# Performance work log

Hardware: AMD Instinct MI355X
Metric: run time of the kernel (lower is better)

Reference implementation:

```python
import jax, jax.numpy as jnp
import numpy as np

SCORE_THRESHOLD = 0.01
NMS_THRESHOLD = 0.5
MAX_DETECTIONS = 100
PRE_NMS_TOPK = 200  # candidates kept per class before NMS (>= MAX_DETECTIONS)


def setup_inputs() -> dict:
    key = jax.random.key(0)
    kc, kcls, kw, kr, kt = jax.random.split(key, 5)
    B, N, C, R = 16, 100000, 30, 3
    # Build valid (x1,y1,x2,y2) boxes: random centers in a 512x512 image, sizes in [1,101].
    cxy = jax.random.uniform(kc, (B, N, 2), dtype=jnp.float32) * 512.0
    wh = jax.random.uniform(kw, (B, N, 2), dtype=jnp.float32) * 100.0 + 1.0
    boxes = jnp.concatenate([cxy - 0.5 * wh, cxy + 0.5 * wh], axis=-1)  # [B,N,4]
    classification = jax.random.uniform(kcls, (B, N, C), dtype=jnp.float32)
    rotation = jax.random.normal(kr, (B, N, R), dtype=jnp.float32)
    translation = jax.random.normal(kt, (B, N, 3), dtype=jnp.float32)
    return {"boxes": boxes, "classification": classification,
            "rotation": rotation, "translation": translation}


def _iou_matrix(b):  # b: [K,4] -> [K,K] pairwise IoU
    x1, y1, x2, y2 = b[:, 0], b[:, 1], b[:, 2], b[:, 3]
    area = jnp.maximum(x2 - x1, 0.0) * jnp.maximum(y2 - y1, 0.0)
    xx1 = jnp.maximum(x1[:, None], x1[None, :])
    yy1 = jnp.maximum(y1[:, None], y1[None, :])
    xx2 = jnp.minimum(x2[:, None], x2[None, :])
    yy2 = jnp.minimum(y2[:, None], y2[None, :])
    inter = jnp.maximum(xx2 - xx1, 0.0) * jnp.maximum(yy2 - yy1, 0.0)
    union = area[:, None] + area[None, :] - inter
    return inter / jnp.maximum(union, 1e-8)


def _nms_one_class(scores, boxes):
    # scores: [N], boxes: [N,4] -> (kept_scores [K], source_indices [K])
    masked = jnp.where(scores > SCORE_THRESHOLD, scores, -jnp.inf)
    top_s, top_i = jax.lax.top_k(masked, PRE_NMS_TOPK)
    cand = boxes[top_i]                      # [K,4], already sorted by score desc
    iou = _iou_matrix(cand)                  # [K,K]
    valid = jnp.isfinite(top_s)
    rng = jnp.arange(PRE_NMS_TOPK)

    def body(i, keep):
        suppress = (iou[i] > NMS_THRESHOLD) & (rng > i) & keep[i]
        return keep & ~suppress

    keep = jax.lax.fori_loop(0, PRE_NMS_TOPK, body, valid)
    return jnp.where(keep, top_s, -jnp.inf), top_i


def reference(boxes, classification, rotation, translation):
    B, N, C = classification.shape

    def per_image(bx, cls, rot, tr):
        # Per-class score threshold + NMS, vectorized over classes.
        s, idx = jax.vmap(lambda c: _nms_one_class(cls[:, c], bx))(jnp.arange(C))
        labels = jnp.broadcast_to(jnp.arange(C)[:, None], s.shape)
        s, idx, labels = s.reshape(-1), idx.reshape(-1), labels.reshape(-1)
        # Global top-k over all (class, kept-box) pairs.
        top_s, sel = jax.lax.top_k(s, MAX_DETECTIONS)
        fidx, flab = idx[sel], labels[sel]
        valid = jnp.isfinite(top_s)
        out_boxes = jnp.where(valid[:, None], bx[fidx], -1.0)
        out_scores = jnp.where(valid, top_s, -1.0)
        out_labels = jnp.where(valid, flab, -1).astype(jnp.int32)
        out_rot = jnp.where(valid[:, None], rot[fidx], -1.0)
        out_tr = jnp.where(valid[:, None], tr[fidx], -1.0)
        return out_boxes, out_scores, out_labels, out_rot, out_tr

    return jax.vmap(per_image)(boxes, classification, rotation, translation)
```

## Files before the change

### kernel.cpp

```cpp
#include <hip/hip_runtime.h>
#include <math.h>

typedef unsigned long long u64;

#define BATCH 16
#define NBOX 100000
#define NCLS 30
#define K 200
#define MAXDET 100
#define SCORE_THR 0.01f
#define NMS_THR 0.5f
#define T0 0.995f

#define ELEM_PER_BATCH (NBOX * NCLS)
#define CAP 1024
#define CHUNKS 48
#define VEC_PER_CHUNK 15625
#define LDS_CAP 48

#define OFF_COLL   0ull
#define OFF_CNT    (OFF_COLL + (size_t)BATCH*NCLS*CAP*8)
#define OFF_WSI    (OFF_CNT + 512*4)
#define OFF_MERGE  (OFF_WSI + (size_t)BATCH*NCLS*K*4)

__global__ __launch_bounds__(512) void collect_kernel(const float* __restrict__ cls,
                                                      int* __restrict__ cnt,
                                                      u64* __restrict__ coll) {
  const int b = blockIdx.x / CHUNKS;
  const int chunk = blockIdx.x % CHUNKS;
  const int tid = threadIdx.x;

  __shared__ u64 lbuf[NCLS][LDS_CAP];
  __shared__ int lcnt[NCLS];
  __shared__ int lbase[NCLS];

  if (tid < NCLS) lcnt[tid] = 0;
  __syncthreads();

  const int vbase = chunk * VEC_PER_CHUNK;
  const float4* p = (const float4*)(cls + (size_t)b * ELEM_PER_BATCH) + vbase;
  for (int i = tid; i < VEC_PER_CHUNK; i += 512) {
    float4 v = p[i];
    float m = fmaxf(fmaxf(v.x, v.y), fmaxf(v.z, v.w));
    if (m > T0) {
      float vv[4] = {v.x, v.y, v.z, v.w};
      #pragma unroll
      for (int j = 0; j < 4; ++j) {
        float f = vv[j];
        if (f > T0) {
          int e = (vbase + i) * 4 + j;
          int c = e % NCLS;
          int n = e / NCLS;
          int pos = atomicAdd(&lcnt[c], 1);
          if (pos < LDS_CAP)
            lbuf[c][pos] = ((u64)__float_as_uint(f) << 32) | (unsigned)(~(unsigned)n);
        }
      }
    }
  }
  __syncthreads();

  if (tid < NCLS) {
    int m = lcnt[tid];
    int stored = (m < LDS_CAP) ? m : LDS_CAP;
    int bump = (m > LDS_CAP) ? 1000000 : 0;
    int base = atomicAdd(&cnt[b * NCLS + tid], m + bump);
    lbase[tid] = base;
    lcnt[tid] = stored;
  }
  __syncthreads();

  for (int t = tid; t < NCLS * LDS_CAP; t += 512) {
    int c = t / LDS_CAP, s = t - (t / LDS_CAP) * LDS_CAP;
    if (s < lcnt[c]) {
      int slot = lbase[c] + s;
      if (slot < CAP)
        coll[(size_t)(b * NCLS + c) * CAP + slot] = lbuf[c][s];
    }
  }
}

__global__ __launch_bounds__(512) void fused_sort_nms_kernel(
    const u64* __restrict__ coll, const int* __restrict__ cnt,
    const float* __restrict__ cls, const float* __restrict__ boxes,
    int* __restrict__ ws_i, u64* __restrict__ merged) {
  const int bc = blockIdx.x;
  const int b = bc / NCLS, c = bc % NCLS;
  const int tid = threadIdx.x;

  __shared__ u64 arr[CAP];
  __shared__ float sx1[K], sy1[K], sx2[K], sy2[K], sarea[K], ss[K];
  __shared__ int sidx[K];
  __shared__ unsigned mask[K][8];
  __shared__ unsigned keepw[8];
  __shared__ int s_surv;
  __shared__ u64 comb[256];
  __shared__ unsigned eqbuf[512];
  __shared__ unsigned s_pref, s_mask, s_krem, s_takeall;
  __shared__ unsigned s_cntgt, s_cnteq;

  const int ct = cnt[bc];
  const bool bad = (ct < K) || (ct > CAP);
  if (!bad) {
    for (int i = tid; i < CAP; i += 512)
      arr[i] = (i < ct) ? coll[(size_t)bc * CAP + i] : 0ull;
    for (int k = 2; k <= CAP; k <<= 1) {
      for (int j = k >> 1; j > 0; j >>= 1) {
        __syncthreads();
        for (int i = tid; i < CAP; i += 512) {
          int l = i ^ j;
          if (l > i) {
            u64 a = arr[i], bb = arr[l];
            bool up = ((i & k) == 0);
            if (up ? (a < bb) : (a > bb)) { arr[i] = bb; arr[l] = a; }
          }
        }
      }
    }
    __syncthreads();
    for (int r = tid; r < K; r += 512) {
      u64 e = arr[r];
      float s = (e != 0ull) ? __uint_as_float((unsigned)(e >> 32)) : -INFINITY;
      int idx = (e != 0ull) ? (int)(~(unsigned)e) : 0;
      ss[r] = s; sidx[r] = idx;
      ws_i[bc * K + r] = idx;
    }
  } else {
    unsigned (*hist)[256] = (unsigned (*)[256])arr;
    const int wv = tid >> 6;
    if (tid == 0) { s_pref = 0u; s_mask = 0u; s_krem = K; s_takeall = 0u; }
    __syncthreads();
    const float* col = cls + (size_t)b * NBOX * NCLS + c;

    for (int pass = 0; pass < 4; ++pass) {
      if (s_takeall) break;
      const int shift = 24 - 8 * pass;
      for (int i = tid; i < 8 * 256; i += 512) ((unsigned*)hist)[i] = 0u;
      __syncthreads();
      const unsigned pref = s_pref, msk = s_mask;
      for (int n = tid; n < NBOX; n += 512) {
        float v = col[(size_t)n * NCLS];
        if (v > SCORE_THR) {
          unsigned key = __float_as_uint(v);
          if ((key & msk) == pref)
            atomicAdd(&hist[wv][(key >> shift) & 0xFFu], 1u);
        }
      }
      __syncthreads();
      if (tid < 256) {
        unsigned t2 = 0;
        for (int w = 0; w < 8; ++w) t2 += hist[w][tid];
        hist[0][tid] = t2;
      }
      __syncthreads();
      if (tid == 0) {
        unsigned krem = s_krem, cum = 0; int dsel = -1;
        for (int d = 255; d >= 0; --d) {
          unsigned cc = hist[0][d];
          if (cum + cc >= krem) { dsel = d; break; }
          cum += cc;
        }
        if (dsel < 0) s_takeall = 1u;
        else {
          s_krem = krem - cum;
          s_pref = pref | ((unsigned)dsel << shift);
          s_mask = msk | (0xFFu << shift);
        }
      }
      __syncthreads();
    }

    if (tid == 0) { s_cntgt = 0u; s_cnteq = 0u; }
    __syncthreads();
    const unsigned pivot = s_pref;
    const unsigned takeall = s_takeall;

    for (int n = tid; n < NBOX; n += 512) {
      float v = col[(size_t)n * NCLS];
      if (v > SCORE_THR) {
        unsigned key = __float_as_uint(v);
        if (takeall || key > pivot) {
          unsigned pos = atomicAdd(&s_cntgt, 1u);
          if (pos < 256u)
            comb[pos] = ((u64)key << 32) | (unsigned)(~(unsigned)n);
        } else if (key == pivot) {
          unsigned pos = atomicAdd(&s_cnteq, 1u);
          if (pos < 512u) eqbuf[pos] = (unsigned)n;
        }
      }
    }
    __syncthreads();
    const unsigned cntgt = (s_cntgt < 256u) ? s_cntgt : 256u;
    const unsigned cnteq = (s_cnteq < 512u) ? s_cnteq : 512u;
    unsigned need = 0;
    if (!takeall) {
      need = (cntgt < (unsigned)K) ? ((unsigned)K - cntgt) : 0u;
      if (need > cnteq) need = cnteq;
    }
    for (int i = tid; i < 512; i += 512)
      if ((unsigned)i >= cnteq) eqbuf[i] = 0xFFFFFFFFu;
    for (int k = 2; k <= 512; k <<= 1) {
      for (int j = k >> 1; j > 0; j >>= 1) {
        __syncthreads();
        {
          int i = tid, l = i ^ j;
          if (l > i) {
            unsigned a = eqbuf[i], bb = eqbuf[l];
            bool up = ((i & k) == 0);
            if (up ? (a > bb) : (a < bb)) { eqbuf[i] = bb; eqbuf[l] = a; }
          }
        }
      }
    }
    __syncthreads();
    for (int t = tid; t < (int)need; t += 512)
      comb[cntgt + t] = ((u64)pivot << 32) | (unsigned)(~eqbuf[t]);
    const unsigned M = cntgt + need;
    for (int i = tid; i < 256; i += 512)
      if ((unsigned)i >= M) comb[i] = 0ull;
    for (int k = 2; k <= 256; k <<= 1) {
      for (int j = k >> 1; j > 0; j >>= 1) {
        __syncthreads();
        if (tid < 256) {
          int i = tid, l = i ^ j;
          if (l > i) {
            u64 a = comb[i], bb = comb[l];
            bool up = ((i & k) == 0);
            if (up ? (a < bb) : (a > bb)) { comb[i] = bb; comb[l] = a; }
          }
        }
      }
    }
    __syncthreads();
    if (tid < K) {
      if ((unsigned)tid < M) {
        u64 e = comb[tid];
        ss[tid] = __uint_as_float((unsigned)(e >> 32));
        sidx[tid] = (int)(~(unsigned)e);
      } else {
        ss[tid] = -INFINITY;
        sidx[tid] = 0;
      }
      ws_i[bc * K + tid] = sidx[tid];
    }
  }
  for (int i = tid; i < K * 8; i += 512) ((unsigned*)mask)[i] = 0u;
  if (tid < 8) keepw[tid] = 0u;
  __syncthreads();

  for (int r = tid; r < K; r += 512) {
    float s = ss[r];
    bool valid = (s != -INFINITY);
    float x1 = 0.f, y1 = 0.f, x2 = 0.f, y2 = 0.f;
    if (valid) {
      const float* bp = boxes + ((size_t)b * NBOX + sidx[r]) * 4;
      x1 = bp[0]; y1 = bp[1]; x2 = bp[2]; y2 = bp[3];
      atomicOr(&keepw[r >> 5], 1u << (r & 31));
    }
    sx1[r] = x1; sy1[r] = y1; sx2[r] = x2; sy2[r] = y2;
    sarea[r] = fmaxf(x2 - x1, 0.f) * fmaxf(y2 - y1, 0.f);
  }
  __syncthreads();

  for (int t = tid; t < K * K; t += 512) {
    int i = t / K, j = t - i * K;
    if (j > i) {
      float xx1 = fmaxf(sx1[i], sx1[j]);
      float yy1 = fmaxf(sy1[i], sy1[j]);
      float xx2 = fminf(sx2[i], sx2[j]);
      float yy2 = fminf(sy2[i], sy2[j]);
      float inter = fmaxf(xx2 - xx1, 0.f) * fmaxf(yy2 - yy1, 0.f);
      float uni = sarea[i] + sarea[j] - inter;
      float iou = inter / fmaxf(uni, 1e-8f);
      if (iou > NMS_THR) atomicOr(&mask[i][j >> 5], 1u << (j & 31));
    }
  }
  __syncthreads();

  if (tid < 64) {
    int w = tid & 7;
    unsigned keep = keepw[w];
    for (int i = 0; i < K; ++i) {
      unsigned kw = __shfl(keep, i >> 5, 64);
      if ((kw >> (i & 31)) & 1u)
        keep &= ~mask[i][w];
    }
    if (tid < 8) keepw[tid] = keep;
  }
  __syncthreads();

  for (int r = tid; r < K; r += 512) {
    int w6 = r >> 5, bit = r & 31;
    if ((keepw[w6] >> bit) & 1u) {
      int pos = 0;
      #pragma unroll
      for (int w = 0; w < 7; ++w) {
        unsigned kw = keepw[w];
        if (w < w6) pos += __popc(kw);
        else if (w == w6) pos += __popc(kw & ((1u << bit) - 1u));
      }
      if (pos < 128) {
        unsigned ord = __float_as_uint(ss[r]) | 0x80000000u;
        merged[((size_t)b * 32 + c) * 128 + pos] =
          ((u64)ord << 32) | (unsigned)(~(unsigned)(c * K + r));
      }
    }
  }
  if (tid == 0) {
    int S = 0;
    #pragma unroll
    for (int w = 0; w < 7; ++w) S += __popc(keepw[w]);
    s_surv = S;
  }
  __syncthreads();
  for (int t = s_surv + tid; t < 128; t += 512)
    merged[((size_t)b * 32 + c) * 128 + t] = 0ull;
}

__global__ __launch_bounds__(1024) void merge_gather_kernel(
    const u64* __restrict__ merged, const int* __restrict__ ws_i,
    const float* __restrict__ boxes, const float* __restrict__ rot,
    const float* __restrict__ tr, float* __restrict__ out) {
  const int b = blockIdx.x;
  const int tid = threadIdx.x;
  __shared__ u64 W[4096];

  for (int t = tid; t < 4096; t += 1024) {
    int c = t >> 7, r = t & 127;
    W[t] = (c < NCLS) ? merged[((size_t)b * 32 + c) * 128 + r] : 0ull;
  }
  __syncthreads();

  int active = 4096;
  #pragma unroll
  for (int level = 0; level < 5; ++level) {
    int npairs = active >> 8;
    for (int t = tid; t < npairs * 64; t += 1024) {
      int p = t >> 6, q = t & 63;
      int i1 = p * 256 + 128 + q, i2 = p * 256 + 255 - q;
      u64 a = W[i1]; W[i1] = W[i2]; W[i2] = a;
    }
    __syncthreads();
    for (int j = 128; j > 0; j >>= 1) {
      for (int i = tid; i < active; i += 1024) {
        int l = i ^ j;
        if (l > i) {
          u64 a = W[i], bb = W[l];
          if (a < bb) { W[i] = bb; W[l] = a; }
        }
      }
      __syncthreads();
    }
    int half = active >> 1;
    u64 t0 = 0, t1 = 0;
    if (tid < half) t0 = W[(tid >> 7) * 256 + (tid & 127)];
    int t2i = tid + 1024;
    if (t2i < half) t1 = W[(t2i >> 7) * 256 + (t2i & 127)];
    __syncthreads();
    if (tid < half) W[tid] = t0;
    if (t2i < half) W[t2i] = t1;
    __syncthreads();
    active = half;
  }

  if (tid < MAXDET) {
    u64 key = W[tid];
    bool valid = (key != 0ull);
    float* ob  = out + ((size_t)b * MAXDET + tid) * 4;
    float* os  = out + (size_t)BATCH * MAXDET * 4 + b * MAXDET + tid;
    float* ol  = os + BATCH * MAXDET;
    float* orr = out + (size_t)BATCH * MAXDET * 6 + ((size_t)b * MAXDET + tid) * 3;
    float* ot  = orr + (size_t)BATCH * MAXDET * 3;

    if (valid) {
      unsigned f = ~(unsigned)key;
      int cl = (int)(f / K);
      float sc = __uint_as_float((unsigned)(key >> 32) & 0x7FFFFFFFu);
      int orig = ws_i[(size_t)b * NCLS * K + f];
      const float* bp = boxes + ((size_t)b * NBOX + orig) * 4;
      ob[0] = bp[0]; ob[1] = bp[1]; ob[2] = bp[2]; ob[3] = bp[3];
      *os = sc;
      *ol = (float)cl;
      const float* rp = rot + ((size_t)b * NBOX + orig) * 3;
      orr[0] = rp[0]; orr[1] = rp[1]; orr[2] = rp[2];
      const float* tp = tr + ((size_t)b * NBOX + orig) * 3;
      ot[0] = tp[0]; ot[1] = tp[1]; ot[2] = tp[2];
    } else {
      ob[0] = ob[1] = ob[2] = ob[3] = -1.f;
      *os = -1.f; *ol = -1.f;
      orr[0] = orr[1] = orr[2] = -1.f;
      ot[0] = ot[1] = ot[2] = -1.f;
    }
  }
}

extern "C" void kernel_launch(void* const* d_in, const int* in_sizes, int n_in,
                              void* d_out, int out_size, void* d_ws, size_t ws_size,
                              hipStream_t stream) {
  const float* boxes = (const float*)d_in[0];
  const float* cls   = (const float*)d_in[1];
  const float* rot   = (const float*)d_in[2];
  const float* tr    = (const float*)d_in[3];
  float* out = (float*)d_out;

  char* ws = (char*)d_ws;
  u64*   coll   = (u64*)(ws + OFF_COLL);
  int*   cnt    = (int*)(ws + OFF_CNT);
  int*   ws_i   = (int*)(ws + OFF_WSI);
  u64*   merged = (u64*)(ws + OFF_MERGE);

  hipMemsetAsync(cnt, 0, BATCH * NCLS * sizeof(int), stream);
  collect_kernel<<<BATCH * CHUNKS, 512, 0, stream>>>(cls, cnt, coll);
  fused_sort_nms_kernel<<<BATCH * NCLS, 512, 0, stream>>>(coll, cnt, cls, boxes,
                                                          ws_i, merged);
  merge_gather_kernel<<<BATCH, 1024, 0, stream>>>(merged, ws_i, boxes, rot, tr, out);
}
```

Baseline: 116.0 us.

## Fuse final merge into NMS kernel via last-block counter, restructure IoU loop

```diff
diff --git a/kernel.cpp b/kernel.cpp
--- a/kernel.cpp
+++ b/kernel.cpp
@@ -39,25 +39,33 @@
 
   const int vbase = chunk * VEC_PER_CHUNK;
   const float4* p = (const float4*)(cls + (size_t)b * ELEM_PER_BATCH) + vbase;
-  for (int i = tid; i < VEC_PER_CHUNK; i += 512) {
-    float4 v = p[i];
+
+  auto process = [&](float4 v, int idx) {
     float m = fmaxf(fmaxf(v.x, v.y), fmaxf(v.z, v.w));
     if (m > T0) {
       float vv[4] = {v.x, v.y, v.z, v.w};
       #pragma unroll
       for (int j = 0; j < 4; ++j) {
-        float f = vv[j];
-        if (f > T0) {
-          int e = (vbase + i) * 4 + j;
+        if (vv[j] > T0) {
+          int e = (vbase + idx) * 4 + j;
           int c = e % NCLS;
           int n = e / NCLS;
           int pos = atomicAdd(&lcnt[c], 1);
           if (pos < LDS_CAP)
-            lbuf[c][pos] = ((u64)__float_as_uint(f) << 32) | (unsigned)(~(unsigned)n);
-        }
-      }
-    }
-  }
+            lbuf[c][pos] = ((u64)__float_as_uint(vv[j]) << 32) | (unsigned)(~(unsigned)n);
+        }
+      }
+    }
+  };
+
+  int i = tid;
+  for (; i + 512 < VEC_PER_CHUNK; i += 1024) {
+    float4 a = p[i];
+    float4 b2 = p[i + 512];
+    process(a, i);
+    process(b2, i + 512);
+  }
+  if (i < VEC_PER_CHUNK) process(p[i], i);
   __syncthreads();
 
   if (tid < NCLS) {
@@ -83,19 +91,26 @@
 __global__ __launch_bounds__(512) void fused_sort_nms_kernel(
     const u64* __restrict__ coll, const int* __restrict__ cnt,
     const float* __restrict__ cls, const float* __restrict__ boxes,
-    int* __restrict__ ws_i, u64* __restrict__ merged) {
+    const float* __restrict__ rot, const float* __restrict__ tr,
+    int* __restrict__ ws_i, u64* __restrict__ merged,
+    int* __restrict__ bcnt, float* __restrict__ out) {
   const int bc = blockIdx.x;
   const int b = bc / NCLS, c = bc % NCLS;
   const int tid = threadIdx.x;
 
-  __shared__ u64 arr[CAP];
-  __shared__ float sx1[K], sy1[K], sx2[K], sy2[K], sarea[K], ss[K];
-  __shared__ int sidx[K];
-  __shared__ unsigned mask[K][8];
+  __shared__ char pool[32768] __attribute__((aligned(16)));
+  u64*      arr   = (u64*)pool;
+  float4*   sbox  = (float4*)(pool + 8192);
+  float*    sarea = (float*)(pool + 11392);
+  float*    ss    = (float*)(pool + 12192);
+  int*      sidx  = (int*)(pool + 12992);
+  unsigned (*mask)[8] = (unsigned (*)[8])(pool + 13792);
+  u64*      comb  = (u64*)(pool + 20192);
+  unsigned* eqbuf = (unsigned*)(pool + 22240);
+  u64*      W     = (u64*)pool;
+
   __shared__ unsigned keepw[8];
-  __shared__ int s_surv;
-  __shared__ u64 comb[256];
-  __shared__ unsigned eqbuf[512];
+  __shared__ int s_surv, s_last;
   __shared__ unsigned s_pref, s_mask, s_krem, s_takeall;
   __shared__ unsigned s_cntgt, s_cnteq;
 
@@ -204,7 +219,7 @@
         __syncthreads();
         {
           int i = tid, l = i ^ j;
-          if (l > i) {
+          if (l > i && i < 512) {
             unsigned a = eqbuf[i], bb = eqbuf[l];
             bool up = ((i & k) == 0);
             if (up ? (a > bb) : (a < bb)) { eqbuf[i] = bb; eqbuf[l] = a; }
@@ -244,6 +259,7 @@
       ws_i[bc * K + tid] = sidx[tid];
     }
   }
+
   for (int i = tid; i < K * 8; i += 512) ((unsigned*)mask)[i] = 0u;
   if (tid < 8) keepw[tid] = 0u;
   __syncthreads();
@@ -257,22 +273,35 @@
       x1 = bp[0]; y1 = bp[1]; x2 = bp[2]; y2 = bp[3];
       atomicOr(&keepw[r >> 5], 1u << (r & 31));
     }
-    sx1[r] = x1; sy1[r] = y1; sx2[r] = x2; sy2[r] = y2;
+    sbox[r] = make_float4(x1, y1, x2, y2);
     sarea[r] = fmaxf(x2 - x1, 0.f) * fmaxf(y2 - y1, 0.f);
   }
   __syncthreads();
 
-  for (int t = tid; t < K * K; t += 512) {
-    int i = t / K, j = t - i * K;
-    if (j > i) {
-      float xx1 = fmaxf(sx1[i], sx1[j]);
-      float yy1 = fmaxf(sy1[i], sy1[j]);
-      float xx2 = fminf(sx2[i], sx2[j]);
-      float yy2 = fminf(sy2[i], sy2[j]);
-      float inter = fmaxf(xx2 - xx1, 0.f) * fmaxf(yy2 - yy1, 0.f);
-      float uni = sarea[i] + sarea[j] - inter;
-      float iou = inter / fmaxf(uni, 1e-8f);
-      if (iou > NMS_THR) atomicOr(&mask[i][j >> 5], 1u << (j & 31));
+  {
+    const int jj = tid & 255;
+    const bool jvalid = (jj < K);
+    float jx1 = 0.f, jy1 = 0.f, jx2 = 0.f, jy2 = 0.f, ja = 0.f;
+    if (jvalid) {
+      float4 jb = sbox[jj];
+      jx1 = jb.x; jy1 = jb.y; jx2 = jb.z; jy2 = jb.w;
+      ja = sarea[jj];
+    }
+    #pragma unroll 4
+    for (int k2 = 0; k2 < K / 2; ++k2) {
+      int i = (tid >> 8) + 2 * k2;
+      float4 ib = sbox[i];
+      float ia = sarea[i];
+      if (jvalid && jj > i) {
+        float xx1 = fmaxf(ib.x, jx1);
+        float yy1 = fmaxf(ib.y, jy1);
+        float xx2 = fminf(ib.z, jx2);
+        float yy2 = fminf(ib.w, jy2);
+        float inter = fmaxf(xx2 - xx1, 0.f) * fmaxf(yy2 - yy1, 0.f);
+        float uni = ia + ja - inter;
+        float iou = inter / fmaxf(uni, 1e-8f);
+        if (iou > NMS_THR) atomicOr(&mask[i][jj >> 5], 1u << (jj & 31));
+      }
     }
   }
   __syncthreads();
@@ -315,34 +344,32 @@
   __syncthreads();
   for (int t = s_surv + tid; t < 128; t += 512)
     merged[((size_t)b * 32 + c) * 128 + t] = 0ull;
-}
-
-__global__ __launch_bounds__(1024) void merge_gather_kernel(
-    const u64* __restrict__ merged, const int* __restrict__ ws_i,
-    const float* __restrict__ boxes, const float* __restrict__ rot,
-    const float* __restrict__ tr, float* __restrict__ out) {
-  const int b = blockIdx.x;
-  const int tid = threadIdx.x;
-  __shared__ u64 W[4096];
-
-  for (int t = tid; t < 4096; t += 1024) {
-    int c = t >> 7, r = t & 127;
-    W[t] = (c < NCLS) ? merged[((size_t)b * 32 + c) * 128 + r] : 0ull;
+
+  __syncthreads();
+  __threadfence();
+  if (tid == 0)
+    s_last = (atomicAdd(&bcnt[b], 1) == NCLS - 1) ? 1 : 0;
+  __syncthreads();
+  if (!s_last) return;
+  __threadfence();
+
+  for (int t = tid; t < 4096; t += 512) {
+    int c2 = t >> 7, r = t & 127;
+    W[t] = (c2 < NCLS) ? merged[((size_t)b * 32 + c2) * 128 + r] : 0ull;
   }
   __syncthreads();
 
   int active = 4096;
-  #pragma unroll
   for (int level = 0; level < 5; ++level) {
     int npairs = active >> 8;
-    for (int t = tid; t < npairs * 64; t += 1024) {
+    for (int t = tid; t < npairs * 64; t += 512) {
       int p = t >> 6, q = t & 63;
       int i1 = p * 256 + 128 + q, i2 = p * 256 + 255 - q;
       u64 a = W[i1]; W[i1] = W[i2]; W[i2] = a;
     }
     __syncthreads();
     for (int j = 128; j > 0; j >>= 1) {
-      for (int i = tid; i < active; i += 1024) {
+      for (int i = tid; i < active; i += 512) {
         int l = i ^ j;
         if (l > i) {
           u64 a = W[i], bb = W[l];
@@ -352,13 +379,16 @@
       __syncthreads();
     }
     int half = active >> 1;
-    u64 t0 = 0, t1 = 0;
-    if (tid < half) t0 = W[(tid >> 7) * 256 + (tid & 127)];
-    int t2i = tid + 1024;
-    if (t2i < half) t1 = W[(t2i >> 7) * 256 + (t2i & 127)];
-    __syncthreads();
-    if (tid < half) W[tid] = t0;
-    if (t2i < half) W[t2i] = t1;
+    u64 v0 = 0, v1 = 0, v2 = 0, v3 = 0;
+    { int t = tid;        if (t < half) v0 = W[(t >> 7) * 256 + (t & 127)]; }
+    { int t = tid + 512;  if (t < half) v1 = W[(t >> 7) * 256 + (t & 127)]; }
+    { int t = tid + 1024; if (t < half) v2 = W[(t >> 7) * 256 + (t & 127)]; }
+    { int t = tid + 1536; if (t < half) v3 = W[(t >> 7) * 256 + (t & 127)]; }
+    __syncthreads();
+    { int t = tid;        if (t < half) W[t] = v0; }
+    { int t = tid + 512;  if (t < half) W[t] = v1; }
+    { int t = tid + 1024; if (t < half) W[t] = v2; }
+    { int t = tid + 1536; if (t < half) W[t] = v3; }
     __syncthreads();
     active = half;
   }
@@ -406,12 +436,13 @@
   char* ws = (char*)d_ws;
   u64*   coll   = (u64*)(ws + OFF_COLL);
   int*   cnt    = (int*)(ws + OFF_CNT);
+  int*   bcnt   = cnt + BATCH * NCLS;
   int*   ws_i   = (int*)(ws + OFF_WSI);
   u64*   merged = (u64*)(ws + OFF_MERGE);
 
-  hipMemsetAsync(cnt, 0, BATCH * NCLS * sizeof(int), stream);
+  hipMemsetAsync(cnt, 0, 512 * sizeof(int), stream);
   collect_kernel<<<BATCH * CHUNKS, 512, 0, stream>>>(cls, cnt, coll);
   fused_sort_nms_kernel<<<BATCH * NCLS, 512, 0, stream>>>(coll, cnt, cls, boxes,
-                                                          ws_i, merged);
-  merge_gather_kernel<<<BATCH, 1024, 0, stream>>>(merged, ws_i, boxes, rot, tr, out);
+                                                          rot, tr, ws_i, merged,
+                                                          bcnt, out);
 }
```

Result: slower. 175.7 us (+51.5%).
